# Performance work log

Measured on AMD Instinct MI355X. Metric: run time of the kernel, lower is better.

## Reference

```python
import jax, jax.numpy as jnp
import numpy as np

N = 200000          # total instances
NUM_BAGS = 25000    # ragged bags, avg size 8
D = 690             # repre_size
R = 53              # rel_size


def setup_inputs() -> dict:
    key = jax.random.key(0)
    k1, k2, k3 = jax.random.split(key, 3)
    repre = jax.random.normal(k1, (N, D), dtype=jnp.float32)
    relation_mat = jax.random.normal(k2, (R, D), dtype=jnp.float32) * 0.001
    bias = jnp.zeros((R,), dtype=jnp.float32)
    labels = jax.random.randint(k3, (N,), 0, R, dtype=jnp.int64)
    # ragged contiguous scopes partitioning [0, N)
    rng = np.random.default_rng(0)
    cuts = np.sort(rng.choice(np.arange(1, N), size=NUM_BAGS - 1, replace=False))
    starts = np.concatenate([[0], cuts])
    ends = np.concatenate([cuts, [N]])
    scope = jnp.asarray(np.stack([starts, ends], axis=1), dtype=jnp.int64)
    return {"repre": repre, "relation_mat": relation_mat, "bias": bias,
            "scope": scope, "labels": labels}


def reference(repre, relation_mat, bias, scope, labels):
    # training / use_bag path of AttentionSelector.forward
    starts = scope[:, 0]
    # segment id for each instance (scopes are a contiguous partition)
    seg = jnp.searchsorted(starts, jnp.arange(N), side="right") - 1  # [N]
    rel_vecs = relation_mat[labels]                      # [N, D]
    rel_logits = jnp.sum(repre * rel_vecs, axis=-1)      # [N]
    # segment softmax (numerically stable)
    m = jax.ops.segment_max(rel_logits, seg, num_segments=NUM_BAGS)
    e = jnp.exp(rel_logits - m[seg])
    denom = jax.ops.segment_sum(e, seg, num_segments=NUM_BAGS)
    w = e / denom[seg]                                   # [N]
    att_repres = jax.ops.segment_sum(w[:, None] * repre, seg,
                                     num_segments=NUM_BAGS)  # [NUM_BAGS, D]
    logits = att_repres @ relation_mat.T + bias          # [NUM_BAGS, R]
    return logits
```

## Files before the change

### kernel.cpp

```cpp
#include <hip/hip_runtime.h>


#define NBAGS  25000
#define DDIM   690
#define D2     345
#define RREL   53
#define WAVES  4
#define BLOCK  256
#define CHUNK  8
#define WIN    64
#define NEG_INF (-3.402823466e38f)

static __device__ __forceinline__ int imin(int a, int b) { return a < b ? a : b; }

__global__ __launch_bounds__(BLOCK, 3) void bag_attn_kernel(
    const float* __restrict__ repre,
    const float* __restrict__ rel,
    const float* __restrict__ bias,
    const int*   __restrict__ scope,
    const int*   __restrict__ labels,
    float*       __restrict__ out)
{
    __shared__ float s_att[WAVES * DDIM];

    const int tid  = threadIdx.x;
    const int lane = tid & 63;
    const int wave = tid >> 6;
    const int bag  = blockIdx.x * WAVES + wave;

    const int start = scope[2 * bag];
    const int end   = scope[2 * bag + 1];

    const float2* rel2 = (const float2*)rel;

    float2 acc[6];
    #pragma unroll
    for (int k = 0; k < 6; ++k) acc[k] = make_float2(0.f, 0.f);
    float m = NEG_INF;
    float l = 0.f;

    for (int w0 = start; w0 < end; w0 += WIN) {
        const int labv = labels[imin(w0 + lane, end - 1)];
        const int wend = imin(w0 + WIN, end);

        for (int row = w0; row < wend; row += CHUNK) {
            const int nc = end - row;

            float2 v[CHUNK][6];
            #pragma unroll
            for (int i = 0; i < CHUNK; ++i) {
                const int rc = imin(row + i, end - 1);
                const float2* rp = (const float2*)(repre + (size_t)rc * DDIM);
                #pragma unroll
                for (int k = 0; k < 6; ++k) {
                    const int f = lane + 64 * k;
                    v[i][k] = (f < D2) ? rp[f] : make_float2(0.f, 0.f);
                }
            }

            float dot[CHUNK];
            #pragma unroll
            for (int i = 0; i < CHUNK; ++i) {
                const int lab = __shfl(labv, row - w0 + i, 64);
                const float2* rl = rel2 + (size_t)lab * D2;
                float d = 0.f;
                #pragma unroll
                for (int k = 0; k < 6; ++k) {
                    const int f = lane + 64 * k;
                    if (f < D2) {
                        const float2 u = rl[f];
                        d = fmaf(v[i][k].x, u.x, fmaf(v[i][k].y, u.y, d));
                    }
                }
                dot[i] = d;
            }

            #pragma unroll
            for (int o = 32; o; o >>= 1) {
                #pragma unroll
                for (int i = 0; i < CHUNK; ++i)
                    dot[i] += __shfl_xor(dot[i], o, 64);
            }

            #pragma unroll
            for (int i = 0; i < CHUNK; ++i)
                if (i >= nc) dot[i] = NEG_INF;

            float bm = dot[0];
            #pragma unroll
            for (int i = 1; i < CHUNK; ++i) bm = fmaxf(bm, dot[i]);
            const float nm = fmaxf(m, bm);
            const float sc = __expf(m - nm);

            float e[CHUNK];
            float es = 0.f;
            #pragma unroll
            for (int i = 0; i < CHUNK; ++i) {
                e[i] = __expf(dot[i] - nm);
                es  += e[i];
            }
            l = fmaf(l, sc, es);

            #pragma unroll
            for (int k = 0; k < 6; ++k) {
                float ax = acc[k].x * sc;
                float ay = acc[k].y * sc;
                #pragma unroll
                for (int i = 0; i < CHUNK; ++i) {
                    ax = fmaf(e[i], v[i][k].x, ax);
                    ay = fmaf(e[i], v[i][k].y, ay);
                }
                acc[k].x = ax;
                acc[k].y = ay;
            }
            m = nm;
        }
    }

    const float inv = 1.f / l;
    float2* satt2 = (float2*)(s_att + wave * DDIM);
    #pragma unroll
    for (int k = 0; k < 6; ++k) {
        const int f = lane + 64 * k;
        if (f < D2) satt2[f] = make_float2(acc[k].x * inv, acc[k].y * inv);
    }
    __syncthreads();

    const int bag0 = blockIdx.x * WAVES;
    for (int r = wave; r < RREL; r += WAVES) {
        const float2* rl = rel2 + (size_t)r * D2;
        float2 u[6];
        #pragma unroll
        for (int k = 0; k < 6; ++k) {
            const int f = lane + 64 * k;
            u[k] = (f < D2) ? rl[f] : make_float2(0.f, 0.f);
        }
        const float b = bias[r];
        #pragma unroll
        for (int g = 0; g < WAVES; ++g) {
            const float2* a2 = (const float2*)(s_att + g * DDIM);
            float dot = 0.f;
            #pragma unroll
            for (int k = 0; k < 6; ++k) {
                const int f = lane + 64 * k;
                if (f < D2) {
                    const float2 a = a2[f];
                    dot = fmaf(u[k].x, a.x, fmaf(u[k].y, a.y, dot));
                }
            }
            #pragma unroll
            for (int o = 32; o; o >>= 1) dot += __shfl_xor(dot, o, 64);
            if (lane == 0) out[(size_t)(bag0 + g) * RREL + r] = dot + b;
        }
    }
}

extern "C" void kernel_launch(void* const* d_in, const int* in_sizes, int n_in,
                              void* d_out, int out_size, void* d_ws, size_t ws_size,
                              hipStream_t stream)
{
    const float* repre  = (const float*)d_in[0];
    const float* rel    = (const float*)d_in[1];
    const float* bias   = (const float*)d_in[2];
    const int*   scope  = (const int*)d_in[3];
    const int*   labels = (const int*)d_in[4];
    float*       out    = (float*)d_out;

    const int grid = NBAGS / WAVES;
    bag_attn_kernel<<<grid, BLOCK, 0, stream>>>(repre, rel, bias, scope, labels, out);
}
```

Measured before the change: 901.8 us.

## Split logit computation into separate kernel and use two-pass segment softmax

Adds a prepass kernel that computes per-row attention logits into workspace. The bag kernel then runs an exact two-pass softmax over those precomputed logits and accumulates the normalized weighted sum without online rescaling or relation-row gathers. This removes the dot-product and rescaling work from the main streaming loop, at the cost of reading the large repre matrix twice and an extra kernel launch. The occupancy hint of the bag kernel is also lowered.

```diff
diff --git a/kernel.cpp b/kernel.cpp
--- a/kernel.cpp
+++ b/kernel.cpp
@@ -1,24 +1,58 @@
 #include <hip/hip_runtime.h>
 
 
+#define NROWS  200000
 #define NBAGS  25000
 #define DDIM   690
 #define D2     345
 #define RREL   53
+#define NEG_INF (-3.402823466e38f)
+
+static __device__ __forceinline__ int imin(int a, int b) { return a < b ? a : b; }
+
+#define L_WAVES 8
+#define L_BLOCK 512
+
+__global__ __launch_bounds__(L_BLOCK, 4) void logit_kernel(
+    const float* __restrict__ repre,
+    const float* __restrict__ rel,
+    const int*   __restrict__ labels,
+    float*       __restrict__ logits)
+{
+    const int lane = threadIdx.x & 63;
+    const int wave = threadIdx.x >> 6;
+    const int row  = blockIdx.x * L_WAVES + wave;
+
+    const int lab = labels[row];
+    const float2* rp = (const float2*)(repre + (size_t)row * DDIM);
+    const float2* rl = (const float2*)rel + (size_t)lab * D2;
+
+    float d = 0.f;
+    #pragma unroll
+    for (int k = 0; k < 6; ++k) {
+        const int f = lane + 64 * k;
+        if (f < D2) {
+            const float2 a = rp[f];
+            const float2 b = rl[f];
+            d = fmaf(a.x, b.x, fmaf(a.y, b.y, d));
+        }
+    }
+    #pragma unroll
+    for (int o = 32; o; o >>= 1) d += __shfl_xor(d, o, 64);
+    if (lane == 0) logits[row] = d;
+}
+
 #define WAVES  4
 #define BLOCK  256
 #define CHUNK  8
 #define WIN    64
-#define NEG_INF (-3.402823466e38f)
 
-static __device__ __forceinline__ int imin(int a, int b) { return a < b ? a : b; }
-
-__global__ __launch_bounds__(BLOCK, 3) void bag_attn_kernel(
+__global__ __launch_bounds__(BLOCK, 2) void bag_attn_kernel(
     const float* __restrict__ repre,
     const float* __restrict__ rel,
     const float* __restrict__ bias,
     const int*   __restrict__ scope,
-    const int*   __restrict__ labels,
+    const float* __restrict__ logits,
     float*       __restrict__ out)
 {
     __shared__ float s_att[WAVES * DDIM];
@@ -31,21 +65,36 @@
     const int start = scope[2 * bag];
     const int end   = scope[2 * bag + 1];
 
-    const float2* rel2 = (const float2*)rel;
+    float m = NEG_INF;
+    float l = 0.f;
+    for (int w0 = start; w0 < end; w0 += WIN) {
+        const int idx = w0 + lane;
+        float lg = logits[imin(idx, end - 1)];
+        if (idx >= end) lg = NEG_INF;
+        float wm = lg;
+        #pragma unroll
+        for (int o = 32; o; o >>= 1) wm = fmaxf(wm, __shfl_xor(wm, o, 64));
+        const float nm = fmaxf(m, wm);
+        const float e  = __expf(lg - nm);
+        float s = e;
+        #pragma unroll
+        for (int o = 32; o; o >>= 1) s += __shfl_xor(s, o, 64);
+        l = fmaf(l, __expf(m - nm), s);
+        m = nm;
+    }
+    const float inv = 1.f / l;
 
     float2 acc[6];
     #pragma unroll
     for (int k = 0; k < 6; ++k) acc[k] = make_float2(0.f, 0.f);
-    float m = NEG_INF;
-    float l = 0.f;
 
     for (int w0 = start; w0 < end; w0 += WIN) {
-        const int labv = labels[imin(w0 + lane, end - 1)];
+        const int idx = w0 + lane;
+        const float lg = logits[imin(idx, end - 1)];
+        const float ev = (idx < end) ? __expf(lg - m) * inv : 0.f;
         const int wend = imin(w0 + WIN, end);
 
         for (int row = w0; row < wend; row += CHUNK) {
-            const int nc = end - row;
-
             float2 v[CHUNK][6];
             #pragma unroll
             for (int i = 0; i < CHUNK; ++i) {
@@ -57,75 +106,33 @@
                     v[i][k] = (f < D2) ? rp[f] : make_float2(0.f, 0.f);
                 }
             }
-
-            float dot[CHUNK];
-            #pragma unroll
-            for (int i = 0; i < CHUNK; ++i) {
-                const int lab = __shfl(labv, row - w0 + i, 64);
-                const float2* rl = rel2 + (size_t)lab * D2;
-                float d = 0.f;
-                #pragma unroll
-                for (int k = 0; k < 6; ++k) {
-                    const int f = lane + 64 * k;
-                    if (f < D2) {
-                        const float2 u = rl[f];
-                        d = fmaf(v[i][k].x, u.x, fmaf(v[i][k].y, u.y, d));
-                    }
-                }
-                dot[i] = d;
-            }
-
-            #pragma unroll
-            for (int o = 32; o; o >>= 1) {
-                #pragma unroll
-                for (int i = 0; i < CHUNK; ++i)
-                    dot[i] += __shfl_xor(dot[i], o, 64);
-            }
-
+            float w[CHUNK];
             #pragma unroll
             for (int i = 0; i < CHUNK; ++i)
-                if (i >= nc) dot[i] = NEG_INF;
-
-            float bm = dot[0];
-            #pragma unroll
-            for (int i = 1; i < CHUNK; ++i) bm = fmaxf(bm, dot[i]);
-            const float nm = fmaxf(m, bm);
-            const float sc = __expf(m - nm);
-
-            float e[CHUNK];
-            float es = 0.f;
-            #pragma unroll
-            for (int i = 0; i < CHUNK; ++i) {
-                e[i] = __expf(dot[i] - nm);
-                es  += e[i];
-            }
-            l = fmaf(l, sc, es);
+                w[i] = __shfl(ev, row - w0 + i, 64);
 
             #pragma unroll
             for (int k = 0; k < 6; ++k) {
-                float ax = acc[k].x * sc;
-                float ay = acc[k].y * sc;
+                float ax = acc[k].x, ay = acc[k].y;
                 #pragma unroll
                 for (int i = 0; i < CHUNK; ++i) {
-                    ax = fmaf(e[i], v[i][k].x, ax);
-                    ay = fmaf(e[i], v[i][k].y, ay);
+                    ax = fmaf(w[i], v[i][k].x, ax);
+                    ay = fmaf(w[i], v[i][k].y, ay);
                 }
-                acc[k].x = ax;
-                acc[k].y = ay;
+                acc[k].x = ax; acc[k].y = ay;
             }
-            m = nm;
         }
     }
 
-    const float inv = 1.f / l;
     float2* satt2 = (float2*)(s_att + wave * DDIM);
     #pragma unroll
     for (int k = 0; k < 6; ++k) {
         const int f = lane + 64 * k;
-        if (f < D2) satt2[f] = make_float2(acc[k].x * inv, acc[k].y * inv);
+        if (f < D2) satt2[f] = acc[k];
     }
     __syncthreads();
 
+    const float2* rel2 = (const float2*)rel;
     const int bag0 = blockIdx.x * WAVES;
     for (int r = wave; r < RREL; r += WAVES) {
         const float2* rl = rel2 + (size_t)r * D2;
@@ -165,7 +172,11 @@
     const int*   scope  = (const int*)d_in[3];
     const int*   labels = (const int*)d_in[4];
     float*       out    = (float*)d_out;
+    float*       logits = (float*)d_ws;
+
+    const int lgrid = NROWS / L_WAVES;
+    logit_kernel<<<lgrid, L_BLOCK, 0, stream>>>(repre, rel, labels, logits);
 
     const int grid = NBAGS / WAVES;
-    bag_attn_kernel<<<grid, BLOCK, 0, stream>>>(repre, rel, bias, scope, labels, out);
+    bag_attn_kernel<<<grid, BLOCK, 0, stream>>>(repre, rel, bias, scope, logits, out);
 }
```

Result: slower. 963.1 us (+6.8%).
